# Optimization experiments

Hardware: AMD Instinct MI355X
Metric: run time of the kernel (lower is better)

Reference implementation:

```python
import jax, jax.numpy as jnp
import numpy as np

B, N, D = 8, 1024, 768
H, Y, M = 12, 64, 3072  # heads, head_dim, hopfield memories (4*D)
STEPS = 12
ALPHA = 0.1
EPS = 1e-5


def setup_inputs() -> dict:
    key = jax.random.key(0)
    k0, k1, k2, k3 = jax.random.split(key, 4)
    return {
        "x": jax.random.normal(k0, (B, N, D), dtype=jnp.float32),
        "gamma": jnp.ones((D,), dtype=jnp.float32),
        "beta_ln": jnp.zeros((D,), dtype=jnp.float32),
        "Wq": jax.random.normal(k1, (H, Y, D), dtype=jnp.float32) / np.float32(np.sqrt(D)),
        "Wk": jax.random.normal(k2, (H, Y, D), dtype=jnp.float32) / np.float32(np.sqrt(D)),
        "xi": jax.random.normal(k3, (M, D), dtype=jnp.float32) / np.float32(np.sqrt(D)),
    }


def _layernorm(x, gamma, beta_ln):
    mu = jnp.mean(x, axis=-1, keepdims=True)
    var = jnp.var(x, axis=-1, keepdims=True)
    return gamma * (x - mu) * jax.lax.rsqrt(var + EPS) + beta_ln


def _energy(g, Wq, Wk, xi):
    # Energy attention: E^ATT = -(1/beta) * sum_{h,q} logsumexp_k(beta * <K_hk, Q_hq>)
    q = jnp.einsum('hyd,bnd->bhny', Wq, g)
    k = jnp.einsum('hyd,bnd->bhny', Wk, g)
    beta = jnp.asarray(1.0 / np.sqrt(Y), g.dtype)
    scores = beta * jnp.einsum('bhky,bhqy->bhkq', k, q)  # [B,H,N_k,N_q]
    e_att = -(1.0 / beta) * jnp.sum(jax.nn.logsumexp(scores, axis=2))
    # Hopfield energy: E^HN = -0.5 * sum relu(g @ xi^T)^2
    h = jnp.einsum('bnd,md->bnm', g, xi)
    e_hn = -0.5 * jnp.sum(jnp.square(jax.nn.relu(h)))
    return e_att + e_hn


def reference(x, gamma, beta_ln, Wq, Wk, xi):
    grad_e = jax.grad(_energy)
    def step(xc, _):
        g = _layernorm(xc, gamma, beta_ln)
        # gradient taken at g (not chained through LayerNorm), then SGD update
        xc = xc - ALPHA * grad_e(g, Wq, Wk, xi)
        return xc, None
    out, _ = jax.lax.scan(step, x, None, length=STEPS)
    return out
```

## Files before the change

kernel.cpp:

```cpp
#include <hip/hip_runtime.h>
#include <math.h>

#define H_ 12
#define STEPS_ 12
#define ALPHA_ 0.1f
#define EPS_ 1e-5f
#define BETA_ 0.125f
#define NTOK 8192

typedef unsigned short u16;
typedef __attribute__((ext_vector_type(8))) u16 u16x8;
typedef __attribute__((ext_vector_type(4))) u16 u16x4;
typedef __attribute__((ext_vector_type(4))) float f32x4;
typedef __attribute__((ext_vector_type(8))) __bf16 bf16x8;

#define MFMA __builtin_amdgcn_mfma_f32_16x16x32_bf16

__device__ __forceinline__ u16 f2bf(float x) {
    unsigned u = __float_as_uint(x);
    u += 0x7FFFu + ((u >> 16) & 1u);
    return (u16)(u >> 16);
}
__device__ __forceinline__ float bf2f(u16 u) {
    return __uint_as_float(((unsigned)u) << 16);
}

__device__ __forceinline__ void gl2lds16(const u16* gsrc, u16* ldst) {
    __builtin_amdgcn_global_load_lds(
        (const __attribute__((address_space(1))) void*)gsrc,
        (__attribute__((address_space(3))) void*)ldst, 16, 0, 0);
}

#define RAW_BARRIER()   asm volatile("s_barrier" ::: "memory")
#define WAIT_VM(n)      asm volatile("s_waitcnt vmcnt(" #n ")" ::: "memory")
#define SCHED_FENCE()   __builtin_amdgcn_sched_barrier(0)

__global__ __launch_bounds__(256) void ln_kernel(const float* __restrict__ x,
    const float* __restrict__ gamma, const float* __restrict__ beta,
    u16* __restrict__ g)
{
    int row = blockIdx.x;
    const float* xr = x + (size_t)row * 768;
    u16* gr = g + (size_t)row * 768;
    int t = threadIdx.x;
    float v0 = xr[t], v1 = xr[t + 256], v2 = xr[t + 512];
    float s = v0 + v1 + v2;
    #pragma unroll
    for (int off = 32; off > 0; off >>= 1) s += __shfl_down(s, off);
    __shared__ float red[8];
    int wid = t >> 6, lane = t & 63;
    if (lane == 0) red[wid] = s;
    __syncthreads();
    if (t == 0) red[0] = (red[0] + red[1] + red[2] + red[3]) * (1.0f / 768.0f);
    __syncthreads();
    float mu = red[0];
    float d0 = v0 - mu, d1 = v1 - mu, d2 = v2 - mu;
    float ss = d0*d0 + d1*d1 + d2*d2;
    #pragma unroll
    for (int off = 32; off > 0; off >>= 1) ss += __shfl_down(ss, off);
    if (lane == 0) red[4 + wid] = ss;
    __syncthreads();
    if (t == 0) red[4] = rsqrtf((red[4] + red[5] + red[6] + red[7]) * (1.0f / 768.0f) + EPS_);
    __syncthreads();
    float rs = red[4];
    gr[t]       = f2bf(gamma[t]       * d0 * rs + beta[t]);
    gr[t + 256] = f2bf(gamma[t + 256] * d1 * rs + beta[t + 256]);
    gr[t + 512] = f2bf(gamma[t + 512] * d2 * rs + beta[t + 512]);
}

__global__ __launch_bounds__(192) void reduce_ln(const u16* __restrict__ part,
    float* __restrict__ xc, const float* __restrict__ gamma,
    const float* __restrict__ beta, u16* __restrict__ g)
{
    int row = blockIdx.x, t = threadIdx.x;
    const u16x4* p0 = (const u16x4*)(part + (size_t)row * 768);
    const u16x4* p1 = (const u16x4*)(part + (size_t)(8192 + row) * 768);
    f32x4* xr = (f32x4*)(xc + (size_t)row * 768);
    f32x4 v = xr[t];
    u16x4 a = p0[t], b = p1[t];
    #pragma unroll
    for (int e = 0; e < 4; ++e) v[e] = fmaf(ALPHA_, bf2f(a[e]) + bf2f(b[e]), v[e]);
    xr[t] = v;
    float s = (v[0] + v[1]) + (v[2] + v[3]);
    #pragma unroll
    for (int off = 32; off > 0; off >>= 1) s += __shfl_down(s, off);
    __shared__ float red[8];
    int wid = t >> 6, lane = t & 63;
    if (lane == 0) red[wid] = s;
    __syncthreads();
    if (t == 0) red[0] = (red[0] + red[1] + red[2]) * (1.0f / 768.0f);
    __syncthreads();
    float mu = red[0];
    f32x4 d;
    #pragma unroll
    for (int e = 0; e < 4; ++e) d[e] = v[e] - mu;
    float ss = (d[0]*d[0] + d[1]*d[1]) + (d[2]*d[2] + d[3]*d[3]);
    #pragma unroll
    for (int off = 32; off > 0; off >>= 1) ss += __shfl_down(ss, off);
    if (lane == 0) red[4 + wid] = ss;
    __syncthreads();
    if (t == 0) red[4] = rsqrtf((red[4] + red[5] + red[6]) * (1.0f / 768.0f) + EPS_);
    __syncthreads();
    float rs = red[4];
    const f32x4 gm = *(const f32x4*)&gamma[t * 4];
    const f32x4 bt = *(const f32x4*)&beta[t * 4];
    u16x4 o;
    #pragma unroll
    for (int e = 0; e < 4; ++e) o[e] = f2bf(fmaf(gm[e], d[e] * rs, bt[e]));
    *(u16x4*)&g[(size_t)row * 768 + t * 4] = o;
}

__global__ __launch_bounds__(256) void convert_bf(const float* __restrict__ src,
                                                  u16* __restrict__ dst, int n4)
{
    int i = blockIdx.x * 256 + threadIdx.x;
    if (i < n4) {
        f32x4 v = *(const f32x4*)&src[i * 4];
        u16x4 o;
        #pragma unroll
        for (int e = 0; e < 4; ++e) o[e] = f2bf(v[e]);
        *(u16x4*)&dst[i * 4] = o;
    }
}

__global__ __launch_bounds__(256) void transpose_bf(const float* __restrict__ Wq,
    const float* __restrict__ Wk, const float* __restrict__ xi, u16* __restrict__ out)
{
    __shared__ float tile[64][65];
    int rb = blockIdx.x * 64, cb = blockIdx.y * 64;
    const float* src;
    if (rb < 768) src = Wq + (size_t)rb * 768;
    else if (rb < 1536) src = Wk + (size_t)(rb - 768) * 768;
    else src = xi + (size_t)(rb - 1536) * 768;
    int t = threadIdx.x;
    #pragma unroll
    for (int it = 0; it < 4; ++it) {
        int r = (t >> 4) + 16 * it;
        f32x4 v = *(const f32x4*)&src[(size_t)r * 768 + cb + (t & 15) * 4];
        #pragma unroll
        for (int e = 0; e < 4; ++e) tile[r][(t & 15) * 4 + e] = v[e];
    }
    __syncthreads();
    #pragma unroll
    for (int it = 0; it < 4; ++it) {
        int cl = (t >> 4) + 16 * it;
        u16x4 o;
        #pragma unroll
        for (int e = 0; e < 4; ++e) o[e] = f2bf(tile[(t & 15) * 4 + e][cl]);
        *(u16x4*)&out[(size_t)(cb + cl) * 4608 + rb + (t & 15) * 4] = o;
    }
}


__global__ __launch_bounds__(512) void gemm_fwd(
    const u16* __restrict__ A,
    const u16* __restrict__ Bt,
    u16* __restrict__ qkb, u16* __restrict__ qkT, u16* __restrict__ midb)
{
    __shared__ __align__(16) u16 S[2][28672];
    const int t = threadIdx.x, w = t >> 6, l = t & 63, g = l >> 4, cid = l & 15;
    const int lr = l & 15, lc = l >> 4;
    const int wm = w >> 2, wn = w & 3;
    const int flat = blockIdx.x;
    const int xcd = flat & 7, slot = flat >> 3;
    const int nid = slot >> 2, mloc = slot & 3;
    const int bm = (xcd * 4 + mloc) * 256;
    const int bn = nid * 192;
    const int NT = 12;

    const u16* aS[4]; int ldA[4];
    #pragma unroll
    for (int j = 0; j < 4; ++j) {
        int rf = 2 * w + (j >> 1), kh = j & 1;
        aS[j] = A + (size_t)(bm + 16 * rf + lr) * 768 + 32 * kh + 8 * lc;
        ldA[j] = rf * 1024 + kh * 512 + l * 8;
    }
    const u16* bS[3]; int ldB[3];
    #pragma unroll
    for (int j = 0; j < 3; ++j) {
        int c = 3 * w + j, rf = c >> 1, kh = c & 1;
        bS[j] = Bt + (size_t)(bn + 16 * rf + lr) * 768 + 32 * kh + 8 * lc;
        ldB[j] = 16384 + rf * 1024 + kh * 512 + l * 8;
    }

    f32x4 acc[8][3] = {};
    bf16x8 afr[4][2], b0[2][2], b1[2];

    #pragma unroll
    for (int j = 0; j < 3; ++j) gl2lds16(bS[j], &S[0][ldB[j]]);
    #pragma unroll
    for (int j = 0; j < 4; ++j) gl2lds16(aS[j], &S[0][ldA[j]]);
    #pragma unroll
    for (int j = 0; j < 3; ++j) gl2lds16(bS[j] + 64, &S[1][ldB[j]]);
    WAIT_VM(3); RAW_BARRIER();

    #pragma unroll 1
    for (int tt = 0; tt < NT; ++tt) {
        const int bf = tt & 1, ob = bf ^ 1;
        const u16* Sa = &S[bf][0];
        const u16* Sb = &S[bf][16384];
        #define LDS_A(ii, hh) (*(const bf16x8*)&Sa[((wm * 8 + (ii)) * 128 + (hh) * 64 + l) * 8])
        #define LDS_B(jj, hh) (*(const bf16x8*)&Sb[((3 * wn + (jj)) * 128 + (hh) * 64 + l) * 8])
        #define MM(ii, jj, BF0, BF1) { \
            acc[ii][jj] = MFMA(afr[(ii) & 3][0], BF0, acc[ii][jj], 0, 0, 0); \
            acc[ii][jj] = MFMA(afr[(ii) & 3][1], BF1, acc[ii][jj], 0, 0, 0); }
        #pragma unroll
        for (int i = 0; i < 4; ++i) { afr[i][0] = LDS_A(i, 0); afr[i][1] = LDS_A(i, 1); }
        #pragma unroll
        for (int j = 0; j < 2; ++j) { b0[j][0] = LDS_B(j, 0); b0[j][1] = LDS_B(j, 1); }
        if (tt + 1 < NT) { gl2lds16(aS[0] + 64 * (tt + 1), &S[ob][ldA[0]]);
                           gl2lds16(aS[1] + 64 * (tt + 1), &S[ob][ldA[1]]); }
        RAW_BARRIER();
        __builtin_amdgcn_s_setprio(1);
        #pragma unroll
        for (int i = 0; i < 4; ++i) { MM(i, 0, b0[0][0], b0[0][1]); MM(i, 1, b0[1][0], b0[1][1]); }
        __builtin_amdgcn_s_setprio(0);
        SCHED_FENCE(); RAW_BARRIER();
        b1[0] = LDS_B(2, 0); b1[1] = LDS_B(2, 1);
        if (tt + 1 < NT) { gl2lds16(aS[2] + 64 * (tt + 1), &S[ob][ldA[2]]);
                           gl2lds16(aS[3] + 64 * (tt + 1), &S[ob][ldA[3]]); }
        RAW_BARRIER();
        __builtin_amdgcn_s_setprio(1);
        #pragma unroll
        for (int i = 0; i < 4; ++i) { MM(i, 2, b1[0], b1[1]); }
        __builtin_amdgcn_s_setprio(0);
        SCHED_FENCE(); RAW_BARRIER();
        #pragma unroll
        for (int i = 0; i < 4; ++i) { afr[i][0] = LDS_A(4 + i, 0); afr[i][1] = LDS_A(4 + i, 1); }
        if (tt + 2 < NT) { gl2lds16(bS[0] + 64 * (tt + 2), &S[bf][ldB[0]]);
                           gl2lds16(bS[1] + 64 * (tt + 2), &S[bf][ldB[1]]); }
        RAW_BARRIER();
        __builtin_amdgcn_s_setprio(1);
        #pragma unroll
        for (int i = 0; i < 4; ++i) { MM(4 + i, 2, b1[0], b1[1]); }
        __builtin_amdgcn_s_setprio(0);
        SCHED_FENCE(); RAW_BARRIER();
        if (tt + 2 < NT) gl2lds16(bS[2] + 64 * (tt + 2), &S[bf][ldB[2]]);
        RAW_BARRIER();
        __builtin_amdgcn_s_setprio(1);
        #pragma unroll
        for (int i = 0; i < 4; ++i) { MM(4 + i, 0, b0[0][0], b0[0][1]); MM(4 + i, 1, b0[1][0], b0[1][1]); }
        __builtin_amdgcn_s_setprio(0);
        SCHED_FENCE();
        if (tt < NT - 2)       { WAIT_VM(3); }
        else if (tt == NT - 2) { WAIT_VM(0); }
        RAW_BARRIER();
        #undef LDS_A
        #undef LDS_B
        #undef MM
    }

    if (bn < 1536) {
        int bidx = bm >> 10;
        #pragma unroll
        for (int i = 0; i < 8; ++i) {
            int tok = bm + wm * 128 + 16 * i + 4 * g;
            #pragma unroll
            for (int j = 0; j < 3; ++j) {
                int col = bn + wn * 48 + 16 * j + cid;
                int sel = col >= 768 ? 1 : 0;
                int cc = col - 768 * sel;
                int hh = cc >> 6, yy = cc & 63;
                u16x4 tv;
                #pragma unroll
                for (int r = 0; r < 4; ++r) {
                    u16 bv = f2bf(acc[i][j][r]);
                    tv[r] = bv;
                    qkb[(size_t)(tok + r) * 1536 + col] = bv;
                }
                *(u16x4*)&qkT[((((size_t)bidx * 12 + hh) * 2 + sel) * 64 + yy) * 1024 + (tok & 1023)] = tv;
            }
        }
    } else {
        #pragma unroll
        for (int i = 0; i < 8; ++i)
            #pragma unroll
            for (int r = 0; r < 4; ++r) {
                size_t row = bm + wm * 128 + 16 * i + 4 * g + r;
                #pragma unroll
                for (int j = 0; j < 3; ++j) {
                    int col = bn + wn * 48 + 16 * j + cid;
                    midb[row * 4608 + col] = f2bf(fmaxf(acc[i][j][r], 0.0f));
                }
            }
    }
}

__global__ __launch_bounds__(512) void gemm_upd(
    const u16* __restrict__ A,
    const u16* __restrict__ Bt,
    u16* __restrict__ part)
{
    __shared__ __align__(16) u16 S[2][28672];
    const int t = threadIdx.x, w = t >> 6, l = t & 63, g = l >> 4, cid = l & 15;
    const int lr = l & 15, lc = l >> 4;
    const int wm = w >> 2, wn = w & 3;
    const int flat = blockIdx.x;
    const int xcd = flat & 7, slot = flat >> 3;
    const int z = slot >> 4, rem = slot & 15;
    const int nid = rem >> 2, mloc = rem & 3;
    const int bm = (xcd * 4 + mloc) * 256, bn = nid * 192;
    const int kbeg = z * 2304;
    const int NT = 36;
    u16* out = part + (size_t)z * 8192 * 768;

    const u16* aS[4]; int ldA[4];
    #pragma unroll
    for (int j = 0; j < 4; ++j) {
        int rf = 2 * w + (j >> 1), kh = j & 1;
        aS[j] = A + (size_t)(bm + 16 * rf + lr) * 4608 + kbeg + 32 * kh + 8 * lc;
        ldA[j] = rf * 1024 + kh * 512 + l * 8;
    }
    const u16* bS[3]; int ldB[3];
    #pragma unroll
    for (int j = 0; j < 3; ++j) {
        int c = 3 * w + j, rf = c >> 1, kh = c & 1;
        bS[j] = Bt + (size_t)(bn + 16 * rf + lr) * 4608 + kbeg + 32 * kh + 8 * lc;
        ldB[j] = 16384 + rf * 1024 + kh * 512 + l * 8;
    }

    f32x4 acc[8][3] = {};
    bf16x8 afr[4][2], b0[2][2], b1[2];

    #pragma unroll
    for (int j = 0; j < 3; ++j) gl2lds16(bS[j], &S[0][ldB[j]]);
    #pragma unroll
    for (int j = 0; j < 4; ++j) gl2lds16(aS[j], &S[0][ldA[j]]);
    #pragma unroll
    for (int j = 0; j < 3; ++j) gl2lds16(bS[j] + 64, &S[1][ldB[j]]);
    WAIT_VM(3); RAW_BARRIER();

    #pragma unroll 1
    for (int tt = 0; tt < NT; ++tt) {
        const int bf = tt & 1, ob = bf ^ 1;
        const u16* Sa = &S[bf][0];
        const u16* Sb = &S[bf][16384];
        #define LDS_A(ii, hh) (*(const bf16x8*)&Sa[((wm * 8 + (ii)) * 128 + (hh) * 64 + l) * 8])
        #define LDS_B(jj, hh) (*(const bf16x8*)&Sb[((3 * wn + (jj)) * 128 + (hh) * 64 + l) * 8])
        #define MM(ii, jj, BF0, BF1) { \
            acc[ii][jj] = MFMA(afr[(ii) & 3][0], BF0, acc[ii][jj], 0, 0, 0); \
            acc[ii][jj] = MFMA(afr[(ii) & 3][1], BF1, acc[ii][jj], 0, 0, 0); }
        #pragma unroll
        for (int i = 0; i < 4; ++i) { afr[i][0] = LDS_A(i, 0); afr[i][1] = LDS_A(i, 1); }
        #pragma unroll
        for (int j = 0; j < 2; ++j) { b0[j][0] = LDS_B(j, 0); b0[j][1] = LDS_B(j, 1); }
        if (tt + 1 < NT) { gl2lds16(aS[0] + 64 * (tt + 1), &S[ob][ldA[0]]);
                           gl2lds16(aS[1] + 64 * (tt + 1), &S[ob][ldA[1]]); }
        RAW_BARRIER();
        __builtin_amdgcn_s_setprio(1);
        #pragma unroll
        for (int i = 0; i < 4; ++i) { MM(i, 0, b0[0][0], b0[0][1]); MM(i, 1, b0[1][0], b0[1][1]); }
        __builtin_amdgcn_s_setprio(0);
        SCHED_FENCE(); RAW_BARRIER();
        b1[0] = LDS_B(2, 0); b1[1] = LDS_B(2, 1);
        if (tt + 1 < NT) { gl2lds16(aS[2] + 64 * (tt + 1), &S[ob][ldA[2]]);
                           gl2lds16(aS[3] + 64 * (tt + 1), &S[ob][ldA[3]]); }
        RAW_BARRIER();
        __builtin_amdgcn_s_setprio(1);
        #pragma unroll
        for (int i = 0; i < 4; ++i) { MM(i, 2, b1[0], b1[1]); }
        __builtin_amdgcn_s_setprio(0);
        SCHED_FENCE(); RAW_BARRIER();
        #pragma unroll
        for (int i = 0; i < 4; ++i) { afr[i][0] = LDS_A(4 + i, 0); afr[i][1] = LDS_A(4 + i, 1); }
        if (tt + 2 < NT) { gl2lds16(bS[0] + 64 * (tt + 2), &S[bf][ldB[0]]);
                           gl2lds16(bS[1] + 64 * (tt + 2), &S[bf][ldB[1]]); }
        RAW_BARRIER();
        __builtin_amdgcn_s_setprio(1);
        #pragma unroll
        for (int i = 0; i < 4; ++i) { MM(4 + i, 2, b1[0], b1[1]); }
        __builtin_amdgcn_s_setprio(0);
        SCHED_FENCE(); RAW_BARRIER();
        if (tt + 2 < NT) gl2lds16(bS[2] + 64 * (tt + 2), &S[bf][ldB[2]]);
        RAW_BARRIER();
        __builtin_amdgcn_s_setprio(1);
        #pragma unroll
        for (int i = 0; i < 4; ++i) { MM(4 + i, 0, b0[0][0], b0[0][1]); MM(4 + i, 1, b0[1][0], b0[1][1]); }
        __builtin_amdgcn_s_setprio(0);
        SCHED_FENCE();
        if (tt < NT - 2)       { WAIT_VM(3); }
        else if (tt == NT - 2) { WAIT_VM(0); }
        RAW_BARRIER();
        #undef LDS_A
        #undef LDS_B
        #undef MM
    }

    #pragma unroll
    for (int i = 0; i < 8; ++i)
        #pragma unroll
        for (int r = 0; r < 4; ++r) {
            size_t row = bm + wm * 128 + 16 * i + 4 * g + r;
            #pragma unroll
            for (int j = 0; j < 3; ++j)
                out[row * 768 + bn + wn * 48 + 16 * j + cid] = f2bf(acc[i][j][r]);
        }
}

__global__ __launch_bounds__(256) void dq_kernel(const u16* __restrict__ qk,
    const u16* __restrict__ qkT, float* __restrict__ L, u16* __restrict__ mid)
{
    const int flat = blockIdx.x;
    const int xcd = flat & 7, slot = flat >> 3;
    const int bh = xcd * 12 + slot / 8;
    const int q0 = (slot % 8) << 7;
    const int b = bh / H_, h = bh % H_;
    const u16* qbase = qk + (size_t)b * 1024 * 1536 + h * 64;
    const u16* kbase = qbase + 768;
    const u16* ktg = qkT + ((size_t)bh * 2 + 1) * 64 * 1024;
    __shared__ __align__(16) u16 KB[2][8192];
    __shared__ __align__(16) u16 Ps[8192];
    const int t = threadIdx.x, w = t >> 6, l = t & 63, g = l >> 4, cid = l & 15;
    const int lr = l & 15, lc = l >> 4;

    #pragma unroll
    for (int h2 = 0; h2 < 2; ++h2)
        #pragma unroll
        for (int ch = 0; ch < 2; ++ch)
            gl2lds16(&qbase[(size_t)(q0 + 32 * w + 16 * h2 + lr) * 1536 + 32 * ch + 8 * lc],
                     &KB[0][(128 * (2 * w + h2) + 64 * ch + l) * 8]);
    __syncthreads();
    bf16x8 QF[2][2];
    #pragma unroll
    for (int jj = 0; jj < 2; ++jj)
        #pragma unroll
        for (int hh = 0; hh < 2; ++hh)
            QF[jj][hh] = *(const bf16x8*)&KB[0][(128 * (2 * w + jj) + 64 * hh + l) * 8];
    __syncthreads();

    auto stageK = [&](int buf, int kt) {
        #pragma unroll
        for (int ch = 0; ch < 2; ++ch) {
            gl2lds16(&kbase[(size_t)(kt * 64 + 16 * w + lr) * 1536 + 32 * ch + 8 * lc],
                     &KB[buf][(128 * w + 64 * ch + l) * 8]);
            gl2lds16(&ktg[(size_t)(16 * w + lr) * 1024 + kt * 64 + 32 * ch + 8 * lc],
                     &KB[buf][4096 + (128 * w + 64 * ch + l) * 8]);
        }
    };

    f32x4 acc[2][4] = {};
    float lrun[2] = {0.0f, 0.0f};

    stageK(0, 0); stageK(1, 1);
    #pragma unroll 1
    for (int kt = 0; kt < 16; ++kt) {
        if (kt == 15) { WAIT_VM(0); } else { WAIT_VM(4); }
        RAW_BARRIER();
        const int buf = kt & 1;
        const u16* Kn = &KB[buf][0];
        const u16* Kt = &KB[buf][4096];
        f32x4 s[4][2];
        #pragma unroll
        for (int i = 0; i < 4; ++i) {
            bf16x8 a0 = *(const bf16x8*)&Kn[(128 * i + l) * 8];
            bf16x8 a1 = *(const bf16x8*)&Kn[(128 * i + 64 + l) * 8];
            #pragma unroll
            for (int jj = 0; jj < 2; ++jj) {
                f32x4 z = {0.f, 0.f, 0.f, 0.f};
                z = MFMA(a0, QF[jj][0], z, 0, 0, 0);
                z = MFMA(a1, QF[jj][1], z, 0, 0, 0);
                s[i][jj] = z;
            }
        }
        #pragma unroll
        for (int jj = 0; jj < 2; ++jj) {
            float psum = 0.0f;
            #pragma unroll
            for (int i = 0; i < 4; ++i) {
                u16x4 pv;
                #pragma unroll
                for (int r = 0; r < 4; ++r) {
                    float p = __expf(s[i][jj][r] * BETA_);
                    psum += p;
                    pv[r] = f2bf(p);
                }
                *(u16x4*)&Ps[(128 * (2 * w + jj) + 32 * i + 16 * (g >> 1) + cid) * 8 + 4 * (g & 1)] = pv;
            }
            psum += __shfl_xor(psum, 16);
            psum += __shfl_xor(psum, 32);
            lrun[jj] += psum;
        }
        #pragma unroll
        for (int jj = 0; jj < 2; ++jj) {
            bf16x8 p0 = *(const bf16x8*)&Ps[(128 * (2 * w + jj) + l) * 8];
            bf16x8 p1 = *(const bf16x8*)&Ps[(128 * (2 * w + jj) + 64 + l) * 8];
            #pragma unroll
            for (int j = 0; j < 4; ++j) {
                acc[jj][j] = MFMA(p0, *(const bf16x8*)&Kt[(128 * j + l) * 8], acc[jj][j], 0, 0, 0);
                acc[jj][j] = MFMA(p1, *(const bf16x8*)&Kt[(128 * j + 64 + l) * 8], acc[jj][j], 0, 0, 0);
            }
        }
        RAW_BARRIER();
        if (kt + 2 < 16) stageK(buf, kt + 2);
    }
    #pragma unroll
    for (int jj = 0; jj < 2; ++jj) {
        if (g == 0)
            L[(size_t)bh * 1024 + q0 + 32 * w + 16 * jj + cid] = __logf(lrun[jj]);
        float linv = 1.0f / lrun[jj];
        #pragma unroll
        for (int r = 0; r < 4; ++r) {
            float fr = __shfl(linv, 4 * g + r);
            int row = q0 + 32 * w + 16 * jj + 4 * g + r;
            #pragma unroll
            for (int j = 0; j < 4; ++j)
                mid[(size_t)(b * 1024 + row) * 4608 + h * 64 + 16 * j + cid] = f2bf(acc[jj][j][r] * fr);
        }
    }
}

__global__ __launch_bounds__(256) void dk_kernel(const u16* __restrict__ qk,
    const u16* __restrict__ qkT, const float* __restrict__ L, u16* __restrict__ mid)
{
    const int flat = blockIdx.x;
    const int xcd = flat & 7, slot = flat >> 3;
    const int bh = xcd * 12 + slot / 8;
    const int k0 = (slot % 8) << 7;
    const int b = bh / H_, h = bh % H_;
    const u16* qbase = qk + (size_t)b * 1024 * 1536 + h * 64;
    const u16* kbase = qbase + 768;
    const u16* qtg = qkT + ((size_t)bh * 2 + 0) * 64 * 1024;
    __shared__ __align__(16) u16 KB[2][8192];
    __shared__ __align__(16) u16 Ps[8192];
    const int t = threadIdx.x, w = t >> 6, l = t & 63, g = l >> 4, cid = l & 15;
    const int lr = l & 15, lc = l >> 4;

    #pragma unroll
    for (int h2 = 0; h2 < 2; ++h2)
        #pragma unroll
        for (int ch = 0; ch < 2; ++ch)
            gl2lds16(&kbase[(size_t)(k0 + 32 * w + 16 * h2 + lr) * 1536 + 32 * ch + 8 * lc],
                     &KB[0][(128 * (2 * w + h2) + 64 * ch + l) * 8]);
    __syncthreads();
    bf16x8 KF[2][2];
    #pragma unroll
    for (int jj = 0; jj < 2; ++jj)
        #pragma unroll
        for (int hh = 0; hh < 2; ++hh)
            KF[jj][hh] = *(const bf16x8*)&KB[0][(128 * (2 * w + jj) + 64 * hh + l) * 8];
    __syncthreads();

    auto stageQ = [&](int buf, int qt) {
        #pragma unroll
        for (int ch = 0; ch < 2; ++ch) {
            gl2lds16(&qbase[(size_t)(qt * 64 + 16 * w + lr) * 1536 + 32 * ch + 8 * lc],
                     &KB[buf][(128 * w + 64 * ch + l) * 8]);
            gl2lds16(&qtg[(size_t)(16 * w + lr) * 1024 + qt * 64 + 32 * ch + 8 * lc],
                     &KB[buf][4096 + (128 * w + 64 * ch + l) * 8]);
        }
    };

    f32x4 acc[2][4] = {};
    stageQ(0, 0); stageQ(1, 1);
    #pragma unroll 1
    for (int qt = 0; qt < 16; ++qt) {
        if (qt == 15) { WAIT_VM(0); } else { WAIT_VM(4); }
        RAW_BARRIER();
        const int buf = qt & 1;
        const u16* Qn = &KB[buf][0];
        const u16* Qt = &KB[buf][4096];
        #pragma unroll
        for (int i = 0; i < 4; ++i) {
            bf16x8 a0 = *(const bf16x8*)&Qn[(128 * i + l) * 8];
            bf16x8 a1 = *(const bf16x8*)&Qn[(128 * i + 64 + l) * 8];
            f32x4 lv = *(const f32x4*)&L[(size_t)bh * 1024 + qt * 64 + 16 * i + 4 * g];
            #pragma unroll
            for (int jj = 0; jj < 2; ++jj) {
                f32x4 z = {0.f, 0.f, 0.f, 0.f};
                z = MFMA(a0, KF[jj][0], z, 0, 0, 0);
                z = MFMA(a1, KF[jj][1], z, 0, 0, 0);
                u16x4 pv;
                #pragma unroll
                for (int r = 0; r < 4; ++r)
                    pv[r] = f2bf(__expf(fmaf(z[r], BETA_, -lv[r])));
                *(u16x4*)&Ps[(128 * (2 * w + jj) + 32 * i + 16 * (g >> 1) + cid) * 8 + 4 * (g & 1)] = pv;
            }
        }
        #pragma unroll
        for (int jj = 0; jj < 2; ++jj) {
            bf16x8 p0 = *(const bf16x8*)&Ps[(128 * (2 * w + jj) + l) * 8];
            bf16x8 p1 = *(const bf16x8*)&Ps[(128 * (2 * w + jj) + 64 + l) * 8];
            #pragma unroll
            for (int j = 0; j < 4; ++j) {
                acc[jj][j] = MFMA(p0, *(const bf16x8*)&Qt[(128 * j + l) * 8], acc[jj][j], 0, 0, 0);
                acc[jj][j] = MFMA(p1, *(const bf16x8*)&Qt[(128 * j + 64 + l) * 8], acc[jj][j], 0, 0, 0);
            }
        }
        RAW_BARRIER();
        if (qt + 2 < 16) stageQ(buf, qt + 2);
    }
    #pragma unroll
    for (int jj = 0; jj < 2; ++jj)
        #pragma unroll
        for (int r = 0; r < 4; ++r) {
            int row = k0 + 32 * w + 16 * jj + 4 * g + r;
            #pragma unroll
            for (int j = 0; j < 4; ++j)
                mid[(size_t)(b * 1024 + row) * 4608 + 768 + h * 64 + 16 * j + cid] = f2bf(acc[jj][j][r]);
        }
}

extern "C" void kernel_launch(void* const* d_in, const int* in_sizes, int n_in,
                              void* d_out, int out_size, void* d_ws, size_t ws_size,
                              hipStream_t stream)
{
    const float* x     = (const float*)d_in[0];
    const float* gamma = (const float*)d_in[1];
    const float* betap = (const float*)d_in[2];
    const float* Wq    = (const float*)d_in[3];
    const float* Wk    = (const float*)d_in[4];
    const float* xi    = (const float*)d_in[5];
    float* xc = (float*)d_out;

    char* p = (char*)d_ws;
    u16* wcat_bf  = (u16*)p; p += (size_t)4608 * 768 * 2;
    u16* wcatT_bf = (u16*)p; p += (size_t)768 * 4608 * 2;
    u16* g_bf     = (u16*)p; p += (size_t)NTOK * 768 * 2;
    u16* qk_bf    = (u16*)p; p += (size_t)NTOK * 1536 * 2;
    u16* qkT_bf   = (u16*)p; p += (size_t)96 * 2 * 64 * 1024 * 2;
    u16* mid_bf   = (u16*)p; p += (size_t)NTOK * 4608 * 2;
    float* L      = (float*)p; p += (size_t)96 * 1024 * 4;
    u16* part = qk_bf;
    (void)ws_size; (void)in_sizes; (void)n_in; (void)out_size;

    hipMemcpyAsync(xc, x, (size_t)NTOK * 768 * 4, hipMemcpyDeviceToDevice, stream);

    convert_bf<<<576, 256, 0, stream>>>(Wq, wcat_bf, 147456);
    convert_bf<<<576, 256, 0, stream>>>(Wk, wcat_bf + 768 * 768, 147456);
    convert_bf<<<2304, 256, 0, stream>>>(xi, wcat_bf + 2 * 768 * 768, 589824);
    transpose_bf<<<dim3(72, 12), 256, 0, stream>>>(Wq, Wk, xi, wcatT_bf);

    ln_kernel<<<NTOK, 256, 0, stream>>>(x, gamma, betap, g_bf);

    for (int step = 0; step < STEPS_; ++step) {
        gemm_fwd<<<768, 512, 0, stream>>>(
            g_bf, wcat_bf, qk_bf, qkT_bf, mid_bf);
        dq_kernel<<<768, 256, 0, stream>>>(qk_bf, qkT_bf, L, mid_bf);
        dk_kernel<<<768, 256, 0, stream>>>(qk_bf, qkT_bf, L, mid_bf);
        gemm_upd<<<256, 512, 0, stream>>>(mid_bf, wcatT_bf, part);
        reduce_ln<<<NTOK, 192, 0, stream>>>(part, xc, gamma, betap, g_bf);
    }
}
```

Baseline: 3.116 ms.

## Switch forward and update GEMMs to 32x32x16 bf16 MFMA tiles

Replaces the 16x16x32 MFMA micro-tiles in gemm_fwd and gemm_upd with 32x32x16 MFMAs. This changes the LDS staging layout, the warp decomposition (4x2 warps, each owning a 64x96 sub-tile) and the epilogue index mapping. The larger instruction tile is meant to cut LDS fragment reads per FLOP and raise MFMA efficiency. The software pipeline is reshaped into three MFMA phases, which changes register pressure and the barrier pattern.

```diff
diff --git a/kernel.cpp b/kernel.cpp
--- a/kernel.cpp
+++ b/kernel.cpp
@@ -12,9 +12,11 @@
 typedef __attribute__((ext_vector_type(8))) u16 u16x8;
 typedef __attribute__((ext_vector_type(4))) u16 u16x4;
 typedef __attribute__((ext_vector_type(4))) float f32x4;
+typedef __attribute__((ext_vector_type(16))) float f32x16;
 typedef __attribute__((ext_vector_type(8))) __bf16 bf16x8;
 
 #define MFMA __builtin_amdgcn_mfma_f32_16x16x32_bf16
+#define MFMA32 __builtin_amdgcn_mfma_f32_32x32x16_bf16
 
 __device__ __forceinline__ u16 f2bf(float x) {
     unsigned u = __float_as_uint(x);
@@ -158,9 +160,9 @@
     u16* __restrict__ qkb, u16* __restrict__ qkT, u16* __restrict__ midb)
 {
     __shared__ __align__(16) u16 S[2][28672];
-    const int t = threadIdx.x, w = t >> 6, l = t & 63, g = l >> 4, cid = l & 15;
-    const int lr = l & 15, lc = l >> 4;
-    const int wm = w >> 2, wn = w & 3;
+    const int t = threadIdx.x, w = t >> 6, l = t & 63;
+    const int l31 = l & 31, lhi = l >> 5;
+    const int wm = w >> 1, wn = w & 1;
     const int flat = blockIdx.x;
     const int xcd = flat & 7, slot = flat >> 3;
     const int nid = slot >> 2, mloc = slot & 3;
@@ -171,20 +173,19 @@
     const u16* aS[4]; int ldA[4];
     #pragma unroll
     for (int j = 0; j < 4; ++j) {
-        int rf = 2 * w + (j >> 1), kh = j & 1;
-        aS[j] = A + (size_t)(bm + 16 * rf + lr) * 768 + 32 * kh + 8 * lc;
-        ldA[j] = rf * 1024 + kh * 512 + l * 8;
+        aS[j] = A + (size_t)(bm + 32 * w + l31) * 768 + 16 * j + 8 * lhi;
+        ldA[j] = (w * 4 + j) * 512 + l * 8;
     }
     const u16* bS[3]; int ldB[3];
     #pragma unroll
     for (int j = 0; j < 3; ++j) {
-        int c = 3 * w + j, rf = c >> 1, kh = c & 1;
-        bS[j] = Bt + (size_t)(bn + 16 * rf + lr) * 768 + 32 * kh + 8 * lc;
-        ldB[j] = 16384 + rf * 1024 + kh * 512 + l * 8;
-    }
-
-    f32x4 acc[8][3] = {};
-    bf16x8 afr[4][2], b0[2][2], b1[2];
+        int f = 3 * w + j;
+        bS[j] = Bt + (size_t)(bn + 32 * (f >> 2) + l31) * 768 + 16 * (f & 3) + 8 * lhi;
+        ldB[j] = 16384 + f * 512 + l * 8;
+    }
+
+    f32x16 acc[2][3] = {};
+    bf16x8 afr[2][4], bfr[3][4];
 
     #pragma unroll
     for (int j = 0; j < 3; ++j) gl2lds16(bS[j], &S[0][ldB[j]]);
@@ -199,89 +200,94 @@
         const int bf = tt & 1, ob = bf ^ 1;
         const u16* Sa = &S[bf][0];
         const u16* Sb = &S[bf][16384];
-        #define LDS_A(ii, hh) (*(const bf16x8*)&Sa[((wm * 8 + (ii)) * 128 + (hh) * 64 + l) * 8])
-        #define LDS_B(jj, hh) (*(const bf16x8*)&Sb[((3 * wn + (jj)) * 128 + (hh) * 64 + l) * 8])
-        #define MM(ii, jj, BF0, BF1) { \
-            acc[ii][jj] = MFMA(afr[(ii) & 3][0], BF0, acc[ii][jj], 0, 0, 0); \
-            acc[ii][jj] = MFMA(afr[(ii) & 3][1], BF1, acc[ii][jj], 0, 0, 0); }
-        #pragma unroll
-        for (int i = 0; i < 4; ++i) { afr[i][0] = LDS_A(i, 0); afr[i][1] = LDS_A(i, 1); }
-        #pragma unroll
-        for (int j = 0; j < 2; ++j) { b0[j][0] = LDS_B(j, 0); b0[j][1] = LDS_B(j, 1); }
+        #pragma unroll
+        for (int i = 0; i < 2; ++i)
+            #pragma unroll
+            for (int ks = 0; ks < 4; ++ks)
+                afr[i][ks] = *(const bf16x8*)&Sa[((2 * wm + i) * 4 + ks) * 512 + l * 8];
+        #pragma unroll
+        for (int ks = 0; ks < 4; ++ks)
+            bfr[0][ks] = *(const bf16x8*)&Sb[((3 * wn + 0) * 4 + ks) * 512 + l * 8];
         if (tt + 1 < NT) { gl2lds16(aS[0] + 64 * (tt + 1), &S[ob][ldA[0]]);
                            gl2lds16(aS[1] + 64 * (tt + 1), &S[ob][ldA[1]]); }
         RAW_BARRIER();
         __builtin_amdgcn_s_setprio(1);
         #pragma unroll
-        for (int i = 0; i < 4; ++i) { MM(i, 0, b0[0][0], b0[0][1]); MM(i, 1, b0[1][0], b0[1][1]); }
+        for (int ks = 0; ks < 4; ++ks)
+            #pragma unroll
+            for (int i = 0; i < 2; ++i)
+                acc[i][0] = MFMA32(afr[i][ks], bfr[0][ks], acc[i][0], 0, 0, 0);
         __builtin_amdgcn_s_setprio(0);
         SCHED_FENCE(); RAW_BARRIER();
-        b1[0] = LDS_B(2, 0); b1[1] = LDS_B(2, 1);
+        #pragma unroll
+        for (int jj = 1; jj < 3; ++jj)
+            #pragma unroll
+            for (int ks = 0; ks < 4; ++ks)
+                bfr[jj][ks] = *(const bf16x8*)&Sb[((3 * wn + jj) * 4 + ks) * 512 + l * 8];
         if (tt + 1 < NT) { gl2lds16(aS[2] + 64 * (tt + 1), &S[ob][ldA[2]]);
                            gl2lds16(aS[3] + 64 * (tt + 1), &S[ob][ldA[3]]); }
         RAW_BARRIER();
         __builtin_amdgcn_s_setprio(1);
         #pragma unroll
-        for (int i = 0; i < 4; ++i) { MM(i, 2, b1[0], b1[1]); }
+        for (int ks = 0; ks < 4; ++ks)
+            #pragma unroll
+            for (int i = 0; i < 2; ++i)
+                acc[i][1] = MFMA32(afr[i][ks], bfr[1][ks], acc[i][1], 0, 0, 0);
         __builtin_amdgcn_s_setprio(0);
         SCHED_FENCE(); RAW_BARRIER();
-        #pragma unroll
-        for (int i = 0; i < 4; ++i) { afr[i][0] = LDS_A(4 + i, 0); afr[i][1] = LDS_A(4 + i, 1); }
         if (tt + 2 < NT) { gl2lds16(bS[0] + 64 * (tt + 2), &S[bf][ldB[0]]);
-                           gl2lds16(bS[1] + 64 * (tt + 2), &S[bf][ldB[1]]); }
+                           gl2lds16(bS[1] + 64 * (tt + 2), &S[bf][ldB[1]]);
+                           gl2lds16(bS[2] + 64 * (tt + 2), &S[bf][ldB[2]]); }
         RAW_BARRIER();
         __builtin_amdgcn_s_setprio(1);
         #pragma unroll
-        for (int i = 0; i < 4; ++i) { MM(4 + i, 2, b1[0], b1[1]); }
-        __builtin_amdgcn_s_setprio(0);
-        SCHED_FENCE(); RAW_BARRIER();
-        if (tt + 2 < NT) gl2lds16(bS[2] + 64 * (tt + 2), &S[bf][ldB[2]]);
-        RAW_BARRIER();
-        __builtin_amdgcn_s_setprio(1);
-        #pragma unroll
-        for (int i = 0; i < 4; ++i) { MM(4 + i, 0, b0[0][0], b0[0][1]); MM(4 + i, 1, b0[1][0], b0[1][1]); }
+        for (int ks = 0; ks < 4; ++ks)
+            #pragma unroll
+            for (int i = 0; i < 2; ++i)
+                acc[i][2] = MFMA32(afr[i][ks], bfr[2][ks], acc[i][2], 0, 0, 0);
         __builtin_amdgcn_s_setprio(0);
         SCHED_FENCE();
         if (tt < NT - 2)       { WAIT_VM(3); }
         else if (tt == NT - 2) { WAIT_VM(0); }
         RAW_BARRIER();
-        #undef LDS_A
-        #undef LDS_B
-        #undef MM
     }
 
     if (bn < 1536) {
         int bidx = bm >> 10;
         #pragma unroll
-        for (int i = 0; i < 8; ++i) {
-            int tok = bm + wm * 128 + 16 * i + 4 * g;
+        for (int i = 0; i < 2; ++i)
             #pragma unroll
             for (int j = 0; j < 3; ++j) {
-                int col = bn + wn * 48 + 16 * j + cid;
+                int col = bn + 96 * wn + 32 * j + l31;
                 int sel = col >= 768 ? 1 : 0;
                 int cc = col - 768 * sel;
                 int hh = cc >> 6, yy = cc & 63;
-                u16x4 tv;
                 #pragma unroll
-                for (int r = 0; r < 4; ++r) {
-                    u16 bv = f2bf(acc[i][j][r]);
-                    tv[r] = bv;
-                    qkb[(size_t)(tok + r) * 1536 + col] = bv;
+                for (int q = 0; q < 4; ++q) {
+                    int tok = bm + 64 * wm + 32 * i + 8 * q + 4 * lhi;
+                    u16x4 tv;
+                    #pragma unroll
+                    for (int r = 0; r < 4; ++r) {
+                        u16 bv = f2bf(acc[i][j][4 * q + r]);
+                        tv[r] = bv;
+                        qkb[(size_t)(tok + r) * 1536 + col] = bv;
+                    }
+                    *(u16x4*)&qkT[((((size_t)bidx * 12 + hh) * 2 + sel) * 64 + yy) * 1024 + (tok & 1023)] = tv;
                 }
-                *(u16x4*)&qkT[((((size_t)bidx * 12 + hh) * 2 + sel) * 64 + yy) * 1024 + (tok & 1023)] = tv;
             }
-        }
     } else {
         #pragma unroll
-        for (int i = 0; i < 8; ++i)
-            #pragma unroll
-            for (int r = 0; r < 4; ++r) {
-                size_t row = bm + wm * 128 + 16 * i + 4 * g + r;
+        for (int i = 0; i < 2; ++i)
+            #pragma unroll
+            for (int j = 0; j < 3; ++j) {
+                int col = bn + 96 * wn + 32 * j + l31;
                 #pragma unroll
-                for (int j = 0; j < 3; ++j) {
-                    int col = bn + wn * 48 + 16 * j + cid;
-                    midb[row * 4608 + col] = f2bf(fmaxf(acc[i][j][r], 0.0f));
-                }
+                for (int q = 0; q < 4; ++q)
+                    #pragma unroll
+                    for (int r = 0; r < 4; ++r) {
+                        size_t row = bm + 64 * wm + 32 * i + 8 * q + 4 * lhi + r;
+                        midb[row * 4608 + col] = f2bf(fmaxf(acc[i][j][4 * q + r], 0.0f));
+                    }
             }
     }
 }
@@ -292,9 +298,9 @@
     u16* __restrict__ part)
 {
     __shared__ __align__(16) u16 S[2][28672];
-    const int t = threadIdx.x, w = t >> 6, l = t & 63, g = l >> 4, cid = l & 15;
-    const int lr = l & 15, lc = l >> 4;
-    const int wm = w >> 2, wn = w & 3;
+    const int t = threadIdx.x, w = t >> 6, l = t & 63;
+    const int l31 = l & 31, lhi = l >> 5;
+    const int wm = w >> 1, wn = w & 1;
     const int flat = blockIdx.x;
     const int xcd = flat & 7, slot = flat >> 3;
     const int z = slot >> 4, rem = slot & 15;
@@ -307,20 +313,19 @@
     const u16* aS[4]; int ldA[4];
     #pragma unroll
     for (int j = 0; j < 4; ++j) {
-        int rf = 2 * w + (j >> 1), kh = j & 1;
-        aS[j] = A + (size_t)(bm + 16 * rf + lr) * 4608 + kbeg + 32 * kh + 8 * lc;
-        ldA[j] = rf * 1024 + kh * 512 + l * 8;
+        aS[j] = A + (size_t)(bm + 32 * w + l31) * 4608 + kbeg + 16 * j + 8 * lhi;
+        ldA[j] = (w * 4 + j) * 512 + l * 8;
     }
     const u16* bS[3]; int ldB[3];
     #pragma unroll
     for (int j = 0; j < 3; ++j) {
-        int c = 3 * w + j, rf = c >> 1, kh = c & 1;
-        bS[j] = Bt + (size_t)(bn + 16 * rf + lr) * 4608 + kbeg + 32 * kh + 8 * lc;
-        ldB[j] = 16384 + rf * 1024 + kh * 512 + l * 8;
-    }
-
-    f32x4 acc[8][3] = {};
-    bf16x8 afr[4][2], b0[2][2], b1[2];
+        int f = 3 * w + j;
+        bS[j] = Bt + (size_t)(bn + 32 * (f >> 2) + l31) * 4608 + kbeg + 16 * (f & 3) + 8 * lhi;
+        ldB[j] = 16384 + f * 512 + l * 8;
+    }
+
+    f32x16 acc[2][3] = {};
+    bf16x8 afr[2][4], bfr[3][4];
 
     #pragma unroll
     for (int j = 0; j < 3; ++j) gl2lds16(bS[j], &S[0][ldB[j]]);
@@ -335,65 +340,70 @@
         const int bf = tt & 1, ob = bf ^ 1;
         const u16* Sa = &S[bf][0];
         const u16* Sb = &S[bf][16384];
-        #define LDS_A(ii, hh) (*(const bf16x8*)&Sa[((wm * 8 + (ii)) * 128 + (hh) * 64 + l) * 8])
-        #define LDS_B(jj, hh) (*(const bf16x8*)&Sb[((3 * wn + (jj)) * 128 + (hh) * 64 + l) * 8])
-        #define MM(ii, jj, BF0, BF1) { \
-            acc[ii][jj] = MFMA(afr[(ii) & 3][0], BF0, acc[ii][jj], 0, 0, 0); \
-            acc[ii][jj] = MFMA(afr[(ii) & 3][1], BF1, acc[ii][jj], 0, 0, 0); }
-        #pragma unroll
-        for (int i = 0; i < 4; ++i) { afr[i][0] = LDS_A(i, 0); afr[i][1] = LDS_A(i, 1); }
-        #pragma unroll
-        for (int j = 0; j < 2; ++j) { b0[j][0] = LDS_B(j, 0); b0[j][1] = LDS_B(j, 1); }
+        #pragma unroll
+        for (int i = 0; i < 2; ++i)
+            #pragma unroll
+            for (int ks = 0; ks < 4; ++ks)
+                afr[i][ks] = *(const bf16x8*)&Sa[((2 * wm + i) * 4 + ks) * 512 + l * 8];
+        #pragma unroll
+        for (int ks = 0; ks < 4; ++ks)
+            bfr[0][ks] = *(const bf16x8*)&Sb[((3 * wn + 0) * 4 + ks) * 512 + l * 8];
         if (tt + 1 < NT) { gl2lds16(aS[0] + 64 * (tt + 1), &S[ob][ldA[0]]);
                            gl2lds16(aS[1] + 64 * (tt + 1), &S[ob][ldA[1]]); }
         RAW_BARRIER();
         __builtin_amdgcn_s_setprio(1);
         #pragma unroll
-        for (int i = 0; i < 4; ++i) { MM(i, 0, b0[0][0], b0[0][1]); MM(i, 1, b0[1][0], b0[1][1]); }
+        for (int ks = 0; ks < 4; ++ks)
+            #pragma unroll
+            for (int i = 0; i < 2; ++i)
+                acc[i][0] = MFMA32(afr[i][ks], bfr[0][ks], acc[i][0], 0, 0, 0);
         __builtin_amdgcn_s_setprio(0);
         SCHED_FENCE(); RAW_BARRIER();
-        b1[0] = LDS_B(2, 0); b1[1] = LDS_B(2, 1);
+        #pragma unroll
+        for (int jj = 1; jj < 3; ++jj)
+            #pragma unroll
+            for (int ks = 0; ks < 4; ++ks)
+                bfr[jj][ks] = *(const bf16x8*)&Sb[((3 * wn + jj) * 4 + ks) * 512 + l * 8];
         if (tt + 1 < NT) { gl2lds16(aS[2] + 64 * (tt + 1), &S[ob][ldA[2]]);
                            gl2lds16(aS[3] + 64 * (tt + 1), &S[ob][ldA[3]]); }
         RAW_BARRIER();
         __builtin_amdgcn_s_setprio(1);
         #pragma unroll
-        for (int i = 0; i < 4; ++i) { MM(i, 2, b1[0], b1[1]); }
+        for (int ks = 0; ks < 4; ++ks)
+            #pragma unroll
+            for (int i = 0; i < 2; ++i)
+                acc[i][1] = MFMA32(afr[i][ks], bfr[1][ks], acc[i][1], 0, 0, 0);
         __builtin_amdgcn_s_setprio(0);
         SCHED_FENCE(); RAW_BARRIER();
-        #pragma unroll
-        for (int i = 0; i < 4; ++i) { afr[i][0] = LDS_A(4 + i, 0); afr[i][1] = LDS_A(4 + i, 1); }
         if (tt + 2 < NT) { gl2lds16(bS[0] + 64 * (tt + 2), &S[bf][ldB[0]]);
-                           gl2lds16(bS[1] + 64 * (tt + 2), &S[bf][ldB[1]]); }
+                           gl2lds16(bS[1] + 64 * (tt + 2), &S[bf][ldB[1]]);
+                           gl2lds16(bS[2] + 64 * (tt + 2), &S[bf][ldB[2]]); }
         RAW_BARRIER();
         __builtin_amdgcn_s_setprio(1);
         #pragma unroll
-        for (int i = 0; i < 4; ++i) { MM(4 + i, 2, b1[0], b1[1]); }
-        __builtin_amdgcn_s_setprio(0);
-        SCHED_FENCE(); RAW_BARRIER();
-        if (tt + 2 < NT) gl2lds16(bS[2] + 64 * (tt + 2), &S[bf][ldB[2]]);
-        RAW_BARRIER();
-        __builtin_amdgcn_s_setprio(1);
-        #pragma unroll
-        for (int i = 0; i < 4; ++i) { MM(4 + i, 0, b0[0][0], b0[0][1]); MM(4 + i, 1, b0[1][0], b0[1][1]); }
+        for (int ks = 0; ks < 4; ++ks)
+            #pragma unroll
+            for (int i = 0; i < 2; ++i)
+                acc[i][2] = MFMA32(afr[i][ks], bfr[2][ks], acc[i][2], 0, 0, 0);
         __builtin_amdgcn_s_setprio(0);
         SCHED_FENCE();
         if (tt < NT - 2)       { WAIT_VM(3); }
         else if (tt == NT - 2) { WAIT_VM(0); }
         RAW_BARRIER();
-        #undef LDS_A
-        #undef LDS_B
-        #undef MM
-    }
-
-    #pragma unroll
-    for (int i = 0; i < 8; ++i)
-        #pragma unroll
-        for (int r = 0; r < 4; ++r) {
-            size_t row = bm + wm * 128 + 16 * i + 4 * g + r;
-            #pragma unroll
-            for (int j = 0; j < 3; ++j)
-                out[row * 768 + bn + wn * 48 + 16 * j + cid] = f2bf(acc[i][j][r]);
+    }
+
+    #pragma unroll
+    for (int i = 0; i < 2; ++i)
+        #pragma unroll
+        for (int j = 0; j < 3; ++j) {
+            int col = bn + 96 * wn + 32 * j + l31;
+            #pragma unroll
+            for (int q = 0; q < 4; ++q)
+                #pragma unroll
+                for (int r = 0; r < 4; ++r) {
+                    size_t row = bm + 64 * wm + 32 * i + 8 * q + 4 * lhi + r;
+                    out[row * 768 + col] = f2bf(acc[i][j][4 * q + r]);
+                }
         }
 }
 
```

Result: slower. 3.206 ms (+2.9%).
